# Optimization experiments

Measured on AMD Instinct MI355X. Metric: run time of the kernel, lower is better.

## Reference

```python
import jax, jax.numpy as jnp
import numpy as np

NUM_USERS = 50000
EMBED_DIM = 128
NUM_EDGES = 800000


def setup_inputs() -> dict:
    key = jax.random.key(0)
    k1, k2, k3, k4, k5 = jax.random.split(key, 5)
    user_emb = jax.random.normal(k1, (NUM_USERS, EMBED_DIM), dtype=jnp.float32)
    # xavier_uniform init for the square weight
    limit = float(np.sqrt(6.0 / (EMBED_DIM + EMBED_DIM)))
    social_weight = jax.random.uniform(k2, (EMBED_DIM, EMBED_DIM), dtype=jnp.float32,
                                       minval=-limit, maxval=limit)
    rows = jax.random.randint(k3, (NUM_EDGES,), 0, NUM_USERS)  # destination nodes
    cols = jax.random.randint(k4, (NUM_EDGES,), 0, NUM_USERS)  # source nodes
    vals = jax.random.uniform(k5, (NUM_EDGES,), dtype=jnp.float32)  # adjacency weights
    return {"user_emb": user_emb, "social_weight": social_weight,
            "rows": rows, "cols": cols, "vals": vals}


def reference(user_emb, social_weight, rows, cols, vals):
    # weighted_emb = user_emb @ W  (dense GEMM)
    weighted = jnp.matmul(user_emb, social_weight)  # [N, D]
    # neighbor_emb = sparse.mm(adj, weighted): out[i] = sum_{e: rows[e]==i} vals[e] * weighted[cols[e]]
    gathered = weighted[cols] * vals[:, None]  # [E, D]
    neighbor = jax.ops.segment_sum(gathered, rows, num_segments=user_emb.shape[0])  # [N, D]
    # dropout is identity in eval mode; residual add
    return user_emb + neighbor
```

## Files before the change

### kernel.cpp

```cpp
#include <hip/hip_runtime.h>

#define DD 128
#define CAP 64

typedef __attribute__((ext_vector_type(8))) short short8;
typedef __attribute__((ext_vector_type(4))) float f32x4;

static __device__ __forceinline__ unsigned pack_bf16_2(float lo, float hi) {
  return __builtin_amdgcn_perm(__float_as_uint(hi) + 0x8000u,
                               __float_as_uint(lo) + 0x8000u, 0x07060302u);
}
static __device__ __forceinline__ unsigned short f2bf(float f) {
  return (unsigned short)((__float_as_uint(f) + 0x8000u) >> 16);
}
static __device__ __forceinline__ float bf2f(unsigned short h) {
  return __uint_as_float((unsigned)h << 16);
}

__global__ __launch_bounds__(256) void k1_transpose_place(
    const float* __restrict__ W, unsigned short* __restrict__ Wtg,
    const int* __restrict__ rows, const int* __restrict__ cols,
    const float* __restrict__ vals, int* __restrict__ counts,
    int2* __restrict__ spair, int E) {
  const int t = threadIdx.x;
  if (blockIdx.x == 0) {
    const int k0 = (t >> 4) * 8;
    const int n0 = (t & 15) * 8;
    float v[8][8];
#pragma unroll
    for (int kk = 0; kk < 8; ++kk) {
      float4 a = *(const float4*)(W + (k0 + kk) * DD + n0);
      float4 b = *(const float4*)(W + (k0 + kk) * DD + n0 + 4);
      v[kk][0] = a.x; v[kk][1] = a.y; v[kk][2] = a.z; v[kk][3] = a.w;
      v[kk][4] = b.x; v[kk][5] = b.y; v[kk][6] = b.z; v[kk][7] = b.w;
    }
#pragma unroll
    for (int nn = 0; nn < 8; ++nn) {
      uint4 d;
      d.x = pack_bf16_2(v[0][nn], v[1][nn]);
      d.y = pack_bf16_2(v[2][nn], v[3][nn]);
      d.z = pack_bf16_2(v[4][nn], v[5][nn]);
      d.w = pack_bf16_2(v[6][nn], v[7][nn]);
      *(uint4*)(Wtg + (size_t)(n0 + nn) * DD + k0) = d;
    }
  } else {
    const int e = (blockIdx.x - 1) * 256 + t;
    if (e < E) {
      const int row = rows[e];
      const int pos = atomicAdd(&counts[row], 1);
      if (pos < CAP)
        spair[(size_t)row * CAP + pos] = make_int2(cols[e], __float_as_int(vals[e]));
    }
  }
}

#define WTS 136
__global__ __launch_bounds__(256) void k2_gemm(
    const float* __restrict__ U, const unsigned short* __restrict__ Wtg,
    unsigned short* __restrict__ wb, float* __restrict__ out, int N,
    int do_copy) {
  __shared__ unsigned short Wt[DD][WTS];
  const int t = threadIdx.x;

#pragma unroll
  for (int i = 0; i < 8; ++i) {
    const int s = t + 256 * i;
    const int n = s >> 4;
    const int k0 = (s & 15) * 8;
    uint4 d = *(const uint4*)(Wtg + (size_t)n * DD + k0);
    *(uint4*)(&Wt[n][k0]) = d;
  }

  const int blk_row0 = blockIdx.x * 128;
  if (do_copy) {
    const int nrow = min(128, N - blk_row0);
    const float4* U4 = (const float4*)(U + (size_t)blk_row0 * DD);
    float4* O4 = (float4*)(out + (size_t)blk_row0 * DD);
    for (int i = t; i < nrow * 32; i += 256) O4[i] = U4[i];
  }
  __syncthreads();

  const int w = t >> 6;
  const int lane = t & 63;
  const int m = lane & 15;
  const int quad = lane >> 4;
  const int row_base = blk_row0 + w * 32;

  short8 afrag[2][4];
#pragma unroll
  for (int s = 0; s < 2; ++s) {
    const int r = min(row_base + s * 16 + m, N - 1);
    const float* up = U + (size_t)r * DD + quad * 8;
#pragma unroll
    for (int c = 0; c < 4; ++c) {
      float4 x = *(const float4*)(up + c * 32);
      float4 y = *(const float4*)(up + c * 32 + 4);
      union { unsigned u[4]; short8 v; } fr;
      fr.u[0] = pack_bf16_2(x.x, x.y);
      fr.u[1] = pack_bf16_2(x.z, x.w);
      fr.u[2] = pack_bf16_2(y.x, y.y);
      fr.u[3] = pack_bf16_2(y.z, y.w);
      afrag[s][c] = fr.v;
    }
  }

  f32x4 acc[2][8];
#pragma unroll
  for (int s = 0; s < 2; ++s)
#pragma unroll
    for (int ct = 0; ct < 8; ++ct) acc[s][ct] = (f32x4){0.f, 0.f, 0.f, 0.f};

#pragma unroll
  for (int c = 0; c < 4; ++c) {
#pragma unroll
    for (int ct = 0; ct < 8; ++ct) {
      short8 bfrag = *(const short8*)&Wt[ct * 16 + m][c * 32 + quad * 8];
      acc[0][ct] = __builtin_amdgcn_mfma_f32_16x16x32_bf16(
          afrag[0][c], bfrag, acc[0][ct], 0, 0, 0);
      acc[1][ct] = __builtin_amdgcn_mfma_f32_16x16x32_bf16(
          afrag[1][c], bfrag, acc[1][ct], 0, 0, 0);
    }
  }

#pragma unroll
  for (int s = 0; s < 2; ++s) {
    const int rb = row_base + s * 16 + quad * 4;
#pragma unroll
    for (int ct = 0; ct < 8; ++ct) {
#pragma unroll
      for (int reg = 0; reg < 4; ++reg) {
        const int r = rb + reg;
        if (r < N) wb[(size_t)r * DD + ct * 16 + m] = f2bf(acc[s][ct][reg]);
      }
    }
  }
}

__global__ __launch_bounds__(256) void k3_accumulate(
    const int* __restrict__ counts, const int2* __restrict__ spair,
    const unsigned short* __restrict__ wb, const float* __restrict__ U,
    float* __restrict__ out, int N) {
  const int r = blockIdx.x * 4 + (threadIdx.x >> 6);
  if (r >= N) return;
  const int lane = threadIdx.x & 63;

  const ushort2* __restrict__ WB2 = (const ushort2*)wb;
  float2 acc = ((const float2*)U)[(size_t)r * 64 + lane];

  const int cnt = min(counts[r], CAP);
  const int2* __restrict__ lst = spair + (size_t)r * CAP;

  int i = 0;
  for (; i + 8 <= cnt; i += 8) {
    int2 p[8];
#pragma unroll
    for (int j = 0; j < 8; ++j) p[j] = lst[i + j];
    ushort2 a[8];
#pragma unroll
    for (int j = 0; j < 8; ++j) a[j] = WB2[(size_t)p[j].x * 64 + lane];
#pragma unroll
    for (int j = 0; j < 8; ++j) {
      const float v = __int_as_float(p[j].y);
      acc.x = fmaf(v, bf2f(a[j].x), acc.x);
      acc.y = fmaf(v, bf2f(a[j].y), acc.y);
    }
  }
  for (; i + 2 <= cnt; i += 2) {
    const int2 p0 = lst[i];
    const int2 p1 = lst[i + 1];
    const ushort2 a0 = WB2[(size_t)p0.x * 64 + lane];
    const ushort2 a1 = WB2[(size_t)p1.x * 64 + lane];
    const float v0 = __int_as_float(p0.y);
    const float v1 = __int_as_float(p1.y);
    acc.x = fmaf(v0, bf2f(a0.x), acc.x);
    acc.y = fmaf(v0, bf2f(a0.y), acc.y);
    acc.x = fmaf(v1, bf2f(a1.x), acc.x);
    acc.y = fmaf(v1, bf2f(a1.y), acc.y);
  }
  if (i < cnt) {
    const int2 p0 = lst[i];
    const ushort2 a0 = WB2[(size_t)p0.x * 64 + lane];
    const float v0 = __int_as_float(p0.y);
    acc.x = fmaf(v0, bf2f(a0.x), acc.x);
    acc.y = fmaf(v0, bf2f(a0.y), acc.y);
  }

  ((float2*)out)[(size_t)r * 64 + lane] = acc;
}

__global__ __launch_bounds__(256) void scatter_kernel(
    const int* __restrict__ rows, const int* __restrict__ cols,
    const float* __restrict__ vals, const unsigned short* __restrict__ wb,
    float* __restrict__ out, int E) {
  const int tid = blockIdx.x * 256 + threadIdx.x;
  const int e = tid >> 6;
  if (e >= E) return;
  const int lane = tid & 63;

  const int row = rows[e];
  const int col = cols[e];
  const float v = vals[e];

  const ushort2 w = ((const ushort2*)wb)[(size_t)col * 64 + lane];
  float* dst = out + (size_t)row * DD + lane * 2;
  unsafeAtomicAdd(dst, v * bf2f(w.x));
  unsafeAtomicAdd(dst + 1, v * bf2f(w.y));
}

static inline size_t align_up(size_t x, size_t a) { return (x + a - 1) & ~(a - 1); }

extern "C" void kernel_launch(void* const* d_in, const int* in_sizes, int n_in,
                              void* d_out, int out_size, void* d_ws, size_t ws_size,
                              hipStream_t stream) {
  const float* U = (const float*)d_in[0];
  const float* W = (const float*)d_in[1];
  const int* rows = (const int*)d_in[2];
  const int* cols = (const int*)d_in[3];
  const float* vals = (const float*)d_in[4];
  float* out = (float*)d_out;

  const int N = in_sizes[0] / DD;
  const int E = in_sizes[2];
  const int gemmBlocks = (N + 127) / 128;

  char* ws = (char*)d_ws;
  size_t off = 0;
  unsigned short* wb = (unsigned short*)(ws + off);
  off = align_up(off + (size_t)N * DD * sizeof(unsigned short), 16);
  unsigned short* Wtg = (unsigned short*)(ws + off);
  off = align_up(off + (size_t)DD * DD * sizeof(unsigned short), 16);
  int* counts = (int*)(ws + off);
  off = align_up(off + (size_t)N * sizeof(int), 16);
  int2* spair = (int2*)(ws + off);
  off = align_up(off + (size_t)N * CAP * sizeof(int2), 16);
  const bool fast_ok = (off <= ws_size);

  if (fast_ok) {
    hipMemsetAsync(counts, 0, (size_t)N * sizeof(int), stream);
    k1_transpose_place<<<1 + (E + 255) / 256, 256, 0, stream>>>(
        W, Wtg, rows, cols, vals, counts, spair, E);
    k2_gemm<<<gemmBlocks, 256, 0, stream>>>(U, Wtg, wb, out, N, 0);
    k3_accumulate<<<(N + 3) / 4, 256, 0, stream>>>(counts, spair, wb, U, out, N);
  } else {
    k1_transpose_place<<<1, 256, 0, stream>>>(W, Wtg, rows, cols, vals,
                                              (int*)Wtg, (int2*)Wtg, 0);
    k2_gemm<<<gemmBlocks, 256, 0, stream>>>(U, Wtg, wb, out, N, 1);
    const long long total = (long long)E * 64;
    scatter_kernel<<<(int)((total + 255) / 256), 256, 0, stream>>>(
        rows, cols, vals, wb, out, E);
  }
}
```

Baseline: 177.4 us.

## Store edge indices in row buckets and add overflow pass for excess edges

The bucket fill now writes only the 4-byte edge index per slot instead of an 8-byte (col, val) pair, and the per-row capacity drops from 64 to 48. This cuts the scattered write traffic of the placement kernel. Edges past the capacity go to a bounded overflow list, and a new small kernel applies them with atomics, which fixes the silent dropping of high-degree edges the old code allowed. In exchange, the accumulate kernel must do extra indirect loads of cols and vals through the edge index, adding a dependent gather per edge. The overflow list is itself capped at 4096 entries.

```diff
diff --git a/kernel.cpp b/kernel.cpp
--- a/kernel.cpp
+++ b/kernel.cpp
@@ -1,7 +1,8 @@
 #include <hip/hip_runtime.h>
 
 #define DD 128
-#define CAP 64
+#define CAP 48
+#define OVF_MAX 4096
 
 typedef __attribute__((ext_vector_type(8))) short short8;
 typedef __attribute__((ext_vector_type(4))) float f32x4;
@@ -19,9 +20,9 @@
 
 __global__ __launch_bounds__(256) void k1_transpose_place(
     const float* __restrict__ W, unsigned short* __restrict__ Wtg,
-    const int* __restrict__ rows, const int* __restrict__ cols,
-    const float* __restrict__ vals, int* __restrict__ counts,
-    int2* __restrict__ spair, int E) {
+    const int* __restrict__ rows, int* __restrict__ counts,
+    int* __restrict__ sidx, int* __restrict__ ovf_cnt, int* __restrict__ ovf,
+    int E) {
   const int t = threadIdx.x;
   if (blockIdx.x == 0) {
     const int k0 = (t >> 4) * 8;
@@ -48,8 +49,12 @@
     if (e < E) {
       const int row = rows[e];
       const int pos = atomicAdd(&counts[row], 1);
-      if (pos < CAP)
-        spair[(size_t)row * CAP + pos] = make_int2(cols[e], __float_as_int(vals[e]));
+      if (pos < CAP) {
+        sidx[(size_t)row * CAP + pos] = e;
+      } else {
+        const int o = atomicAdd(ovf_cnt, 1);
+        if (o < OVF_MAX) ovf[o] = e;
+      }
     }
   }
 }
@@ -137,7 +142,8 @@
 }
 
 __global__ __launch_bounds__(256) void k3_accumulate(
-    const int* __restrict__ counts, const int2* __restrict__ spair,
+    const int* __restrict__ counts, const int* __restrict__ sidx,
+    const int* __restrict__ cols, const float* __restrict__ vals,
     const unsigned short* __restrict__ wb, const float* __restrict__ U,
     float* __restrict__ out, int N) {
   const int r = blockIdx.x * 4 + (threadIdx.x >> 6);
@@ -148,44 +154,68 @@
   float2 acc = ((const float2*)U)[(size_t)r * 64 + lane];
 
   const int cnt = min(counts[r], CAP);
-  const int2* __restrict__ lst = spair + (size_t)r * CAP;
+  const int* __restrict__ lst = sidx + (size_t)r * CAP;
 
   int i = 0;
   for (; i + 8 <= cnt; i += 8) {
-    int2 p[8];
-#pragma unroll
-    for (int j = 0; j < 8; ++j) p[j] = lst[i + j];
+    int e[8];
+#pragma unroll
+    for (int j = 0; j < 8; ++j) e[j] = lst[i + j];
+    int c[8];
+    float v[8];
+#pragma unroll
+    for (int j = 0; j < 8; ++j) { c[j] = cols[e[j]]; v[j] = vals[e[j]]; }
     ushort2 a[8];
 #pragma unroll
-    for (int j = 0; j < 8; ++j) a[j] = WB2[(size_t)p[j].x * 64 + lane];
+    for (int j = 0; j < 8; ++j) a[j] = WB2[(size_t)c[j] * 64 + lane];
 #pragma unroll
     for (int j = 0; j < 8; ++j) {
-      const float v = __int_as_float(p[j].y);
-      acc.x = fmaf(v, bf2f(a[j].x), acc.x);
-      acc.y = fmaf(v, bf2f(a[j].y), acc.y);
+      acc.x = fmaf(v[j], bf2f(a[j].x), acc.x);
+      acc.y = fmaf(v[j], bf2f(a[j].y), acc.y);
     }
   }
   for (; i + 2 <= cnt; i += 2) {
-    const int2 p0 = lst[i];
-    const int2 p1 = lst[i + 1];
-    const ushort2 a0 = WB2[(size_t)p0.x * 64 + lane];
-    const ushort2 a1 = WB2[(size_t)p1.x * 64 + lane];
-    const float v0 = __int_as_float(p0.y);
-    const float v1 = __int_as_float(p1.y);
+    const int e0 = lst[i], e1 = lst[i + 1];
+    const int c0 = cols[e0], c1 = cols[e1];
+    const float v0 = vals[e0], v1 = vals[e1];
+    const ushort2 a0 = WB2[(size_t)c0 * 64 + lane];
+    const ushort2 a1 = WB2[(size_t)c1 * 64 + lane];
     acc.x = fmaf(v0, bf2f(a0.x), acc.x);
     acc.y = fmaf(v0, bf2f(a0.y), acc.y);
     acc.x = fmaf(v1, bf2f(a1.x), acc.x);
     acc.y = fmaf(v1, bf2f(a1.y), acc.y);
   }
   if (i < cnt) {
-    const int2 p0 = lst[i];
-    const ushort2 a0 = WB2[(size_t)p0.x * 64 + lane];
-    const float v0 = __int_as_float(p0.y);
+    const int e0 = lst[i];
+    const int c0 = cols[e0];
+    const float v0 = vals[e0];
+    const ushort2 a0 = WB2[(size_t)c0 * 64 + lane];
     acc.x = fmaf(v0, bf2f(a0.x), acc.x);
     acc.y = fmaf(v0, bf2f(a0.y), acc.y);
   }
 
   ((float2*)out)[(size_t)r * 64 + lane] = acc;
+}
+
+__global__ __launch_bounds__(256) void k4_overflow(
+    const int* __restrict__ ovf_cnt, const int* __restrict__ ovf,
+    const int* __restrict__ rows, const int* __restrict__ cols,
+    const float* __restrict__ vals, const unsigned short* __restrict__ wb,
+    float* __restrict__ out) {
+  const int nov = min(*ovf_cnt, OVF_MAX);
+  const int wave = (blockIdx.x * 256 + threadIdx.x) >> 6;
+  const int nwaves = gridDim.x * 4;
+  const int lane = threadIdx.x & 63;
+  for (int i = wave; i < nov; i += nwaves) {
+    const int e = ovf[i];
+    const int row = rows[e];
+    const int col = cols[e];
+    const float v = vals[e];
+    const ushort2 w = ((const ushort2*)wb)[(size_t)col * 64 + lane];
+    float* dst = out + (size_t)row * DD + lane * 2;
+    unsafeAtomicAdd(dst, v * bf2f(w.x));
+    unsafeAtomicAdd(dst + 1, v * bf2f(w.y));
+  }
 }
 
 __global__ __launch_bounds__(256) void scatter_kernel(
@@ -230,20 +260,25 @@
   unsigned short* Wtg = (unsigned short*)(ws + off);
   off = align_up(off + (size_t)DD * DD * sizeof(unsigned short), 16);
   int* counts = (int*)(ws + off);
-  off = align_up(off + (size_t)N * sizeof(int), 16);
-  int2* spair = (int2*)(ws + off);
-  off = align_up(off + (size_t)N * CAP * sizeof(int2), 16);
+  int* ovf_cnt = counts + N;
+  off = align_up(off + ((size_t)N + 4) * sizeof(int), 16);
+  int* ovf = (int*)(ws + off);
+  off = align_up(off + (size_t)OVF_MAX * sizeof(int), 16);
+  int* sidx = (int*)(ws + off);
+  off = align_up(off + (size_t)N * CAP * sizeof(int), 16);
   const bool fast_ok = (off <= ws_size);
 
   if (fast_ok) {
-    hipMemsetAsync(counts, 0, (size_t)N * sizeof(int), stream);
+    hipMemsetAsync(counts, 0, ((size_t)N + 1) * sizeof(int), stream);
     k1_transpose_place<<<1 + (E + 255) / 256, 256, 0, stream>>>(
-        W, Wtg, rows, cols, vals, counts, spair, E);
+        W, Wtg, rows, counts, sidx, ovf_cnt, ovf, E);
     k2_gemm<<<gemmBlocks, 256, 0, stream>>>(U, Wtg, wb, out, N, 0);
-    k3_accumulate<<<(N + 3) / 4, 256, 0, stream>>>(counts, spair, wb, U, out, N);
+    k3_accumulate<<<(N + 3) / 4, 256, 0, stream>>>(counts, sidx, cols, vals,
+                                                   wb, U, out, N);
+    k4_overflow<<<16, 256, 0, stream>>>(ovf_cnt, ovf, rows, cols, vals, wb, out);
   } else {
-    k1_transpose_place<<<1, 256, 0, stream>>>(W, Wtg, rows, cols, vals,
-                                              (int*)Wtg, (int2*)Wtg, 0);
+    k1_transpose_place<<<1, 256, 0, stream>>>(W, Wtg, rows, (int*)Wtg,
+                                              (int*)Wtg, (int*)Wtg, (int*)Wtg, 0);
     k2_gemm<<<gemmBlocks, 256, 0, stream>>>(U, Wtg, wb, out, N, 1);
     const long long total = (long long)E * 64;
     scatter_kernel<<<(int)((total + 255) / 256), 256, 0, stream>>>(
```

Result: slower. 211.1 us (+19.0%).

## Partition edge placement by row range and shrink bucket capacity with overflow list

Applied to the files above, without the earlier changes.

The edge-bucketing kernel now stages 2048 edges per block in shared memory and places them in several passes, each handling one 4096-row partition. This keeps the atomic counter and bucket writes of concurrently running blocks within a smaller address range for better cache locality. Bucket capacity drops from 64 to 32 to halve the bucket workspace, and edges beyond capacity go to a global overflow list that the accumulate kernel scans linearly for rows that overflowed. The price is extra passes over shared memory in the placement kernel and a possibly slow overflow scan. Correctness also relies on the overflow count staying under 4096.

```diff
diff --git a/kernel.cpp b/kernel.cpp
--- a/kernel.cpp
+++ b/kernel.cpp
@@ -1,7 +1,10 @@
 #include <hip/hip_runtime.h>
 
 #define DD 128
-#define CAP 64
+#define CAP 32
+#define OVF_MAX 4096
+#define EPB 2048
+#define PSHIFT 12
 
 typedef __attribute__((ext_vector_type(8))) short short8;
 typedef __attribute__((ext_vector_type(4))) float f32x4;
@@ -21,7 +24,8 @@
     const float* __restrict__ W, unsigned short* __restrict__ Wtg,
     const int* __restrict__ rows, const int* __restrict__ cols,
     const float* __restrict__ vals, int* __restrict__ counts,
-    int2* __restrict__ spair, int E) {
+    int2* __restrict__ spair, int* __restrict__ ovf_cnt, int* __restrict__ ovf,
+    int E, int nparts) {
   const int t = threadIdx.x;
   if (blockIdx.x == 0) {
     const int k0 = (t >> 4) * 8;
@@ -43,13 +47,36 @@
       d.w = pack_bf16_2(v[6][nn], v[7][nn]);
       *(uint4*)(Wtg + (size_t)(n0 + nn) * DD + k0) = d;
     }
-  } else {
-    const int e = (blockIdx.x - 1) * 256 + t;
-    if (e < E) {
-      const int row = rows[e];
-      const int pos = atomicAdd(&counts[row], 1);
-      if (pos < CAP)
-        spair[(size_t)row * CAP + pos] = make_int2(cols[e], __float_as_int(vals[e]));
+    return;
+  }
+
+  __shared__ int lrow[EPB];
+  __shared__ int lcol[EPB];
+  __shared__ float lval[EPB];
+
+  const int c0 = (blockIdx.x - 1) * EPB;
+  const int n = min(EPB, E - c0);
+
+  for (int i = t; i < n; i += 256) {
+    lrow[i] = rows[c0 + i];
+    lcol[i] = cols[c0 + i];
+    lval[i] = vals[c0 + i];
+  }
+  __syncthreads();
+
+  for (int p = 0; p < nparts; ++p) {
+    for (int i = t; i < n; i += 256) {
+      const int r = lrow[i];
+      if ((r >> PSHIFT) == p) {
+        const int pos = atomicAdd(&counts[r], 1);
+        if (pos < CAP) {
+          spair[(size_t)r * CAP + pos] =
+              make_int2(lcol[i], __float_as_int(lval[i]));
+        } else {
+          const int o = atomicAdd(ovf_cnt, 1);
+          if (o < OVF_MAX) ovf[o] = c0 + i;
+        }
+      }
     }
   }
 }
@@ -139,7 +166,9 @@
 __global__ __launch_bounds__(256) void k3_accumulate(
     const int* __restrict__ counts, const int2* __restrict__ spair,
     const unsigned short* __restrict__ wb, const float* __restrict__ U,
-    float* __restrict__ out, int N) {
+    const int* __restrict__ rows, const int* __restrict__ cols,
+    const float* __restrict__ vals, const int* __restrict__ ovf_cnt,
+    const int* __restrict__ ovf, float* __restrict__ out, int N) {
   const int r = blockIdx.x * 4 + (threadIdx.x >> 6);
   if (r >= N) return;
   const int lane = threadIdx.x & 63;
@@ -147,7 +176,8 @@
   const ushort2* __restrict__ WB2 = (const ushort2*)wb;
   float2 acc = ((const float2*)U)[(size_t)r * 64 + lane];
 
-  const int cnt = min(counts[r], CAP);
+  const int cnt_raw = counts[r];
+  const int cnt = min(cnt_raw, CAP);
   const int2* __restrict__ lst = spair + (size_t)r * CAP;
 
   int i = 0;
@@ -185,6 +215,19 @@
     acc.y = fmaf(v0, bf2f(a0.y), acc.y);
   }
 
+  if (cnt_raw > CAP) {
+    const int nov = min(*ovf_cnt, OVF_MAX);
+    for (int o = 0; o < nov; ++o) {
+      const int e = ovf[o];
+      if (rows[e] == r) {
+        const float v = vals[e];
+        const ushort2 a = WB2[(size_t)cols[e] * 64 + lane];
+        acc.x = fmaf(v, bf2f(a.x), acc.x);
+        acc.y = fmaf(v, bf2f(a.y), acc.y);
+      }
+    }
+  }
+
   ((float2*)out)[(size_t)r * 64 + lane] = acc;
 }
 
@@ -222,6 +265,8 @@
   const int N = in_sizes[0] / DD;
   const int E = in_sizes[2];
   const int gemmBlocks = (N + 127) / 128;
+  const int nparts = (N + (1 << PSHIFT) - 1) >> PSHIFT;
+  const int CPB = (E + EPB - 1) / EPB;
 
   char* ws = (char*)d_ws;
   size_t off = 0;
@@ -230,20 +275,25 @@
   unsigned short* Wtg = (unsigned short*)(ws + off);
   off = align_up(off + (size_t)DD * DD * sizeof(unsigned short), 16);
   int* counts = (int*)(ws + off);
-  off = align_up(off + (size_t)N * sizeof(int), 16);
+  int* ovf_cnt = counts + N;
+  off = align_up(off + ((size_t)N + 4) * sizeof(int), 16);
+  int* ovf = (int*)(ws + off);
+  off = align_up(off + (size_t)OVF_MAX * sizeof(int), 16);
   int2* spair = (int2*)(ws + off);
   off = align_up(off + (size_t)N * CAP * sizeof(int2), 16);
   const bool fast_ok = (off <= ws_size);
 
   if (fast_ok) {
-    hipMemsetAsync(counts, 0, (size_t)N * sizeof(int), stream);
-    k1_transpose_place<<<1 + (E + 255) / 256, 256, 0, stream>>>(
-        W, Wtg, rows, cols, vals, counts, spair, E);
+    hipMemsetAsync(counts, 0, ((size_t)N + 1) * sizeof(int), stream);
+    k1_transpose_place<<<1 + CPB, 256, 0, stream>>>(
+        W, Wtg, rows, cols, vals, counts, spair, ovf_cnt, ovf, E, nparts);
     k2_gemm<<<gemmBlocks, 256, 0, stream>>>(U, Wtg, wb, out, N, 0);
-    k3_accumulate<<<(N + 3) / 4, 256, 0, stream>>>(counts, spair, wb, U, out, N);
+    k3_accumulate<<<(N + 3) / 4, 256, 0, stream>>>(
+        counts, spair, wb, U, rows, cols, vals, ovf_cnt, ovf, out, N);
   } else {
     k1_transpose_place<<<1, 256, 0, stream>>>(W, Wtg, rows, cols, vals,
-                                              (int*)Wtg, (int2*)Wtg, 0);
+                                              (int*)Wtg, (int2*)Wtg, (int*)Wtg,
+                                              (int*)Wtg, 0, 0);
     k2_gemm<<<gemmBlocks, 256, 0, stream>>>(U, Wtg, wb, out, N, 1);
     const long long total = (long long)E * 64;
     scatter_kernel<<<(int)((total + 255) / 256), 256, 0, stream>>>(
```

Measured after the change: 189.9 us. 7.1% more time.

## Replace global per-row atomics with two-pass bucketed CSR build fused into GEMM

Applied to the files above, without the earlier changes.

Edge placement is restructured into two passes. First, edges are binned by row range into coarse buckets using shared-memory histograms and one global atomic per bucket per block. Then one block per bucket distributes edges to per-row slots with shared-memory atomics; these blocks run in the same launch as the GEMM blocks. This replaces 800k scattered global atomics with mostly LDS atomics and drops the large memset, at the cost of an extra bucket buffer round trip and a linear overflow scan in the accumulate kernel, which gets expensive if overflow entries ever appear.

```diff
diff --git a/kernel.cpp b/kernel.cpp
--- a/kernel.cpp
+++ b/kernel.cpp
@@ -1,7 +1,12 @@
 #include <hip/hip_runtime.h>
 
 #define DD 128
-#define CAP 64
+#define CAP 32
+#define OVF_MAX 4096
+#define EPB 2048
+#define BSHIFT 10
+#define NBKT_MAX 64
+#define BCAP 24576
 
 typedef __attribute__((ext_vector_type(8))) short short8;
 typedef __attribute__((ext_vector_type(4))) float f32x4;
@@ -17,11 +22,12 @@
   return __uint_as_float((unsigned)h << 16);
 }
 
-__global__ __launch_bounds__(256) void k1_transpose_place(
+__global__ __launch_bounds__(256) void p1_bucket(
     const float* __restrict__ W, unsigned short* __restrict__ Wtg,
     const int* __restrict__ rows, const int* __restrict__ cols,
-    const float* __restrict__ vals, int* __restrict__ counts,
-    int2* __restrict__ spair, int E) {
+    const float* __restrict__ vals, int* __restrict__ binctr,
+    int2* __restrict__ bucket, int* __restrict__ ovf_cnt,
+    int4* __restrict__ ovf, int E, int nbkt) {
   const int t = threadIdx.x;
   if (blockIdx.x == 0) {
     const int k0 = (t >> 4) * 8;
@@ -43,35 +49,98 @@
       d.w = pack_bf16_2(v[6][nn], v[7][nn]);
       *(uint4*)(Wtg + (size_t)(n0 + nn) * DD + k0) = d;
     }
-  } else {
-    const int e = (blockIdx.x - 1) * 256 + t;
-    if (e < E) {
-      const int row = rows[e];
-      const int pos = atomicAdd(&counts[row], 1);
-      if (pos < CAP)
-        spair[(size_t)row * CAP + pos] = make_int2(cols[e], __float_as_int(vals[e]));
+    return;
+  }
+
+  __shared__ int lrow[EPB];
+  __shared__ int hist[NBKT_MAX];
+  __shared__ int gbase[NBKT_MAX];
+  __shared__ int lcur[NBKT_MAX];
+
+  const int c0 = (blockIdx.x - 1) * EPB;
+  const int n = min(EPB, E - c0);
+
+  if (t < NBKT_MAX) { hist[t] = 0; lcur[t] = 0; }
+  __syncthreads();
+
+  for (int i = t; i < n; i += 256) {
+    const int r = rows[c0 + i];
+    lrow[i] = r;
+    atomicAdd(&hist[r >> BSHIFT], 1);
+  }
+  __syncthreads();
+
+  if (t < nbkt && hist[t] > 0) gbase[t] = atomicAdd(&binctr[t], hist[t]);
+  __syncthreads();
+
+  for (int i = t; i < n; i += 256) {
+    const int r = lrow[i];
+    const int b = r >> BSHIFT;
+    const int lpos = atomicAdd(&lcur[b], 1);
+    const int idx = gbase[b] + lpos;
+    const int col = cols[c0 + i];
+    const float v = vals[c0 + i];
+    if (idx < BCAP) {
+      bucket[(size_t)b * BCAP + idx] =
+          make_int2(((r & 1023) << 22) | col, __float_as_int(v));
+    } else {
+      const int o = atomicAdd(ovf_cnt, 1);
+      if (o < OVF_MAX) ovf[o] = make_int4(r, col, __float_as_int(v), 0);
     }
   }
 }
 
 #define WTS 136
-__global__ __launch_bounds__(256) void k2_gemm(
+__global__ __launch_bounds__(256) void p2k2_fused(
+    const int* __restrict__ binctr, const int2* __restrict__ bucket,
+    int* __restrict__ counts, int2* __restrict__ spair,
+    int* __restrict__ ovf_cnt, int4* __restrict__ ovf,
     const float* __restrict__ U, const unsigned short* __restrict__ Wtg,
     unsigned short* __restrict__ wb, float* __restrict__ out, int N,
-    int do_copy) {
-  __shared__ unsigned short Wt[DD][WTS];
+    int nbkt, int do_copy) {
+  __shared__ union {
+    unsigned short Wt[DD][WTS];
+    int scnt[1 << BSHIFT];
+  } sm;
   const int t = threadIdx.x;
 
+  if ((int)blockIdx.x < nbkt) {
+    const int b = blockIdx.x;
+    const int base = b << BSHIFT;
+    const int nrows = min(1 << BSHIFT, N - base);
+    for (int i = t; i < (1 << BSHIFT); i += 256) sm.scnt[i] = 0;
+    __syncthreads();
+
+    const int nb = min(binctr[b], BCAP);
+    const int2* __restrict__ bkt = bucket + (size_t)b * BCAP;
+    for (int i = t; i < nb; i += 256) {
+      const int2 p = bkt[i];
+      const int lr = (unsigned)p.x >> 22;
+      const int col = p.x & 0x3FFFFF;
+      const int slot = atomicAdd(&sm.scnt[lr], 1);
+      if (slot < CAP) {
+        spair[(size_t)(base + lr) * CAP + slot] = make_int2(col, p.y);
+      } else {
+        const int o = atomicAdd(ovf_cnt, 1);
+        if (o < OVF_MAX) ovf[o] = make_int4(base + lr, col, p.y, 0);
+      }
+    }
+    __syncthreads();
+    for (int i = t; i < nrows; i += 256) counts[base + i] = sm.scnt[i];
+    return;
+  }
+
+  const int gb = blockIdx.x - nbkt;
 #pragma unroll
   for (int i = 0; i < 8; ++i) {
     const int s = t + 256 * i;
-    const int n = s >> 4;
+    const int nn = s >> 4;
     const int k0 = (s & 15) * 8;
-    uint4 d = *(const uint4*)(Wtg + (size_t)n * DD + k0);
-    *(uint4*)(&Wt[n][k0]) = d;
-  }
-
-  const int blk_row0 = blockIdx.x * 128;
+    uint4 d = *(const uint4*)(Wtg + (size_t)nn * DD + k0);
+    *(uint4*)(&sm.Wt[nn][k0]) = d;
+  }
+
+  const int blk_row0 = gb * 128;
   if (do_copy) {
     const int nrow = min(128, N - blk_row0);
     const float4* U4 = (const float4*)(U + (size_t)blk_row0 * DD);
@@ -114,7 +183,7 @@
   for (int c = 0; c < 4; ++c) {
 #pragma unroll
     for (int ct = 0; ct < 8; ++ct) {
-      short8 bfrag = *(const short8*)&Wt[ct * 16 + m][c * 32 + quad * 8];
+      short8 bfrag = *(const short8*)&sm.Wt[ct * 16 + m][c * 32 + quad * 8];
       acc[0][ct] = __builtin_amdgcn_mfma_f32_16x16x32_bf16(
           afrag[0][c], bfrag, acc[0][ct], 0, 0, 0);
       acc[1][ct] = __builtin_amdgcn_mfma_f32_16x16x32_bf16(
@@ -139,6 +208,7 @@
 __global__ __launch_bounds__(256) void k3_accumulate(
     const int* __restrict__ counts, const int2* __restrict__ spair,
     const unsigned short* __restrict__ wb, const float* __restrict__ U,
+    const int* __restrict__ ovf_cnt, const int4* __restrict__ ovf,
     float* __restrict__ out, int N) {
   const int r = blockIdx.x * 4 + (threadIdx.x >> 6);
   if (r >= N) return;
@@ -185,6 +255,19 @@
     acc.y = fmaf(v0, bf2f(a0.y), acc.y);
   }
 
+  const int nov = min(*ovf_cnt, OVF_MAX);
+  if (nov > 0) {
+    for (int o = 0; o < nov; ++o) {
+      const int4 e = ovf[o];
+      if (e.x == r) {
+        const float v = __int_as_float(e.z);
+        const ushort2 a = WB2[(size_t)e.y * 64 + lane];
+        acc.x = fmaf(v, bf2f(a.x), acc.x);
+        acc.y = fmaf(v, bf2f(a.y), acc.y);
+      }
+    }
+  }
+
   ((float2*)out)[(size_t)r * 64 + lane] = acc;
 }
 
@@ -222,6 +305,8 @@
   const int N = in_sizes[0] / DD;
   const int E = in_sizes[2];
   const int gemmBlocks = (N + 127) / 128;
+  const int nchunks = (E + EPB - 1) / EPB;
+  const int nbkt = (N + (1 << BSHIFT) - 1) >> BSHIFT;
 
   char* ws = (char*)d_ws;
   size_t off = 0;
@@ -231,20 +316,32 @@
   off = align_up(off + (size_t)DD * DD * sizeof(unsigned short), 16);
   int* counts = (int*)(ws + off);
   off = align_up(off + (size_t)N * sizeof(int), 16);
+  int* binctr = (int*)(ws + off);
+  int* ovf_cnt = binctr + NBKT_MAX;
+  off = align_up(off + (NBKT_MAX + 4) * sizeof(int), 16);
+  int4* ovf = (int4*)(ws + off);
+  off = align_up(off + (size_t)OVF_MAX * sizeof(int4), 16);
+  int2* bucket = (int2*)(ws + off);
+  off = align_up(off + (size_t)nbkt * BCAP * sizeof(int2), 16);
   int2* spair = (int2*)(ws + off);
   off = align_up(off + (size_t)N * CAP * sizeof(int2), 16);
-  const bool fast_ok = (off <= ws_size);
+  const bool fast_ok = (off <= ws_size) && (nbkt <= NBKT_MAX);
 
   if (fast_ok) {
-    hipMemsetAsync(counts, 0, (size_t)N * sizeof(int), stream);
-    k1_transpose_place<<<1 + (E + 255) / 256, 256, 0, stream>>>(
-        W, Wtg, rows, cols, vals, counts, spair, E);
-    k2_gemm<<<gemmBlocks, 256, 0, stream>>>(U, Wtg, wb, out, N, 0);
-    k3_accumulate<<<(N + 3) / 4, 256, 0, stream>>>(counts, spair, wb, U, out, N);
+    hipMemsetAsync(binctr, 0, (NBKT_MAX + 1) * sizeof(int), stream);
+    p1_bucket<<<1 + nchunks, 256, 0, stream>>>(
+        W, Wtg, rows, cols, vals, binctr, bucket, ovf_cnt, ovf, E, nbkt);
+    p2k2_fused<<<nbkt + gemmBlocks, 256, 0, stream>>>(
+        binctr, bucket, counts, spair, ovf_cnt, ovf, U, Wtg, wb, out, N,
+        nbkt, 0);
+    k3_accumulate<<<(N + 3) / 4, 256, 0, stream>>>(
+        counts, spair, wb, U, ovf_cnt, ovf, out, N);
   } else {
-    k1_transpose_place<<<1, 256, 0, stream>>>(W, Wtg, rows, cols, vals,
-                                              (int*)Wtg, (int2*)Wtg, 0);
-    k2_gemm<<<gemmBlocks, 256, 0, stream>>>(U, Wtg, wb, out, N, 1);
+    p1_bucket<<<1, 256, 0, stream>>>(W, Wtg, rows, cols, vals, (int*)Wtg,
+                                     (int2*)Wtg, (int*)Wtg, (int4*)Wtg, 0, 0);
+    p2k2_fused<<<gemmBlocks, 256, 0, stream>>>(
+        (const int*)Wtg, (const int2*)Wtg, (int*)Wtg, (int2*)Wtg, (int*)Wtg,
+        (int4*)Wtg, U, Wtg, wb, out, N, 0, 1);
     const long long total = (long long)E * 64;
     scatter_kernel<<<(int)((total + 255) / 256), 256, 0, stream>>>(
         rows, cols, vals, wb, out, E);
```

After: 164.2 us. -7.4%, faster.
